# Optimization experiments

Measured on AMD Instinct MI355X. Metric: run time of the kernel, lower is better.

The kernel has to match this reference:

```python
import jax, jax.numpy as jnp
import numpy as np

HEADS = 24
HEAD_DIM = 128
HIDDEN = HEADS * HEAD_DIM          # 3072
MLP_DIM = int(HIDDEN * 4.0)        # 12288
EPS = 1e-6


def _layernorm(x, eps=EPS):
    mu = jnp.mean(x, axis=-1, keepdims=True)
    var = jnp.mean(jnp.square(x - mu), axis=-1, keepdims=True)
    return (x - mu) * jax.lax.rsqrt(var + eps)


def _rmsnorm(x, w, eps=EPS):
    var = jnp.mean(jnp.square(x), axis=-1, keepdims=True)
    return x * jax.lax.rsqrt(var + eps) * w


def _apply_rope_transposed(x, freqs_cis):
    # x: [B, S_img, H, Dh]; freqs_cis: [S_img, 2*Dh]
    cos, sin = jnp.split(freqs_cis[:, None, :], 2, axis=-1)  # each [S_img, 1, Dh]
    xr = x.reshape(*x.shape[:-1], -1, 2)                      # interleaved pairs
    x_real, x_imag = xr[..., 0], xr[..., 1]
    x_rot = jnp.stack([-x_imag, x_real], axis=-1).reshape(x.shape)
    return x * cos + x_rot * sin


def setup_inputs() -> dict:
    key = jax.random.key(0)
    ks = jax.random.split(key, 20)
    B, S_IMG, S_TXT = 1, 2048, 256
    s = 0.02
    inp = {
        "hidden_states": jax.random.normal(ks[0], (B, S_IMG, HIDDEN), jnp.float32),
        "encoder_hidden_states": jax.random.normal(ks[1], (B, S_TXT, HIDDEN), jnp.float32),
        "temb": jax.random.normal(ks[2], (B, HIDDEN), jnp.float32),
        "freqs_cis": jax.random.uniform(ks[3], (S_IMG, 2 * HEAD_DIM), jnp.float32),
        # AdaLN: Linear(hidden, 3*hidden)
        "w_norm": jax.random.normal(ks[4], (HIDDEN, 3 * HIDDEN), jnp.float32) * s,
        "b_norm": jnp.zeros((3 * HIDDEN,), jnp.float32),
        # attention projections (bias=True)
        "wq": jax.random.normal(ks[5], (HIDDEN, HIDDEN), jnp.float32) * s,
        "bq": jnp.zeros((HIDDEN,), jnp.float32),
        "wk": jax.random.normal(ks[6], (HIDDEN, HIDDEN), jnp.float32) * s,
        "bk": jnp.zeros((HIDDEN,), jnp.float32),
        "wv": jax.random.normal(ks[7], (HIDDEN, HIDDEN), jnp.float32) * s,
        "bv": jnp.zeros((HIDDEN,), jnp.float32),
        # QK RMSNorm weights over head_dim
        "nq_w": jnp.ones((HEAD_DIM,), jnp.float32),
        "nk_w": jnp.ones((HEAD_DIM,), jnp.float32),
        # parallel MLP branch
        "w_mlp": jax.random.normal(ks[8], (HIDDEN, MLP_DIM), jnp.float32) * s,
        "b_mlp": jnp.zeros((MLP_DIM,), jnp.float32),
        # proj_out: Linear(hidden + mlp_dim, hidden)
        "w_out": jax.random.normal(ks[9], (HIDDEN + MLP_DIM, HIDDEN), jnp.float32) * s,
        "b_out": jnp.zeros((HIDDEN,), jnp.float32),
    }
    return inp


def reference(hidden_states, encoder_hidden_states, temb, freqs_cis,
              w_norm, b_norm, wq, bq, wk, bk, wv, bv, nq_w, nk_w,
              w_mlp, b_mlp, w_out, b_out):
    B = hidden_states.shape[0]
    T = encoder_hidden_states.shape[1]  # text_seq_length

    x = jnp.concatenate([hidden_states, encoder_hidden_states], axis=1)  # [B,S,D]
    residual = x

    # AdaLayerNormZeroSingle
    emb = jax.nn.silu(temb) @ w_norm + b_norm          # [B, 3D]
    emb = emb[:, None, :]                              # [B, 1, 3D]
    shift, scale, gate = jnp.split(emb, 3, axis=-1)    # each [B,1,D]
    nx = _layernorm(x) * (1.0 + scale) + shift         # [B,S,D]

    # parallel MLP branch
    mlp = jax.nn.gelu(nx @ w_mlp + b_mlp, approximate=True)  # [B,S,MLP]

    # attention: q/k/v over full (img+txt) normed sequence
    q = (nx @ wq + bq).reshape(B, -1, HEADS, HEAD_DIM)
    k = (nx @ wk + bk).reshape(B, -1, HEADS, HEAD_DIM)
    v = (nx @ wv + bv).reshape(B, -1, HEADS, HEAD_DIM)
    q = _rmsnorm(q, nq_w)
    k = _rmsnorm(k, nk_w)

    # transposed RoPE on image tokens only
    q = jnp.concatenate([_apply_rope_transposed(q[:, :-T], freqs_cis), q[:, -T:]], axis=1)
    k = jnp.concatenate([_apply_rope_transposed(k[:, :-T], freqs_cis), k[:, -T:]], axis=1)

    # full (non-varlen) scaled dot-product attention
    scores = jnp.einsum("bqhd,bkhd->bhqk", q, k) / np.sqrt(HEAD_DIM).astype(np.float32)
    probs = jax.nn.softmax(scores, axis=-1)
    attn = jnp.einsum("bhqk,bkhd->bqhd", probs, v).reshape(B, -1, HIDDEN)

    # concat attention + mlp, project, gated residual
    h = jnp.concatenate([attn, mlp], axis=2)           # [B,S,D+MLP]
    h = gate * (h @ w_out + b_out) + residual          # [B,S,D]

    return h[:, :-T, :], h[:, -T:, :]
```

## Files before the change

### kernel.cpp

```cpp
#include <hip/hip_runtime.h>
#include <hip/hip_bf16.h>

typedef unsigned short u16;
typedef short s16x8 __attribute__((ext_vector_type(8)));
typedef float f32x4 __attribute__((ext_vector_type(4)));
typedef int   i32x4 __attribute__((ext_vector_type(4)));
typedef u16   u16x4 __attribute__((ext_vector_type(4)));
typedef unsigned int u32;
typedef u32   u32x2 __attribute__((ext_vector_type(2)));

#define HEADS  24
#define HD     128
#define HIDDEN 3072
#define MLPD   12288
#define NTOK   2304
#define SIMG   2048
#define NEMB   9216
#define CATD   15360
#define QKVD   9216
#define FUSEN  21504
#define LN_EPS 1e-6f
#define MB     9

__device__ __forceinline__ u16 f2us(float f){
  __hip_bfloat16 h = __float2bfloat16(f);
  return *reinterpret_cast<u16*>(&h);
}
__device__ __forceinline__ float us2f(u16 u){
  __hip_bfloat16 h;
  *reinterpret_cast<u16*>(&h) = u;
  return __bfloat162float(h);
}
__device__ __forceinline__ float gelu_tanh(float x){
  float y = 0.7978845608028654f*(x + 0.044715f*x*x*x);
  y = fminf(fmaxf(y, -12.f), 12.f);
  float e = __expf(-2.f*y);
  float t = (1.f - e) / (1.f + e);
  return 0.5f*x*(1.0f + t);
}
__device__ __forceinline__ void gload16(const u16* g, u16* l){
  __builtin_amdgcn_global_load_lds(
      (const __attribute__((address_space(1))) void*)g,
      (__attribute__((address_space(3))) void*)l, 16, 0, 0);
}
#define BAR() do{ asm volatile("":::"memory"); __builtin_amdgcn_s_barrier(); asm volatile("":::"memory"); }while(0)
#define LGKM0() asm volatile("s_waitcnt lgkmcnt(0)":::"memory")
#define VMW_(n) asm volatile("s_waitcnt vmcnt(" #n ")":::"memory")
#define VMW(n) VMW_(n)

__global__ __launch_bounds__(256)
void emb_partial(const float* __restrict__ temb, const float* __restrict__ wn,
                 float* __restrict__ partial)
{
  __shared__ float ls[384];
  int tid = threadIdx.x;
  int kb = blockIdx.y * 384;
  for (int i = tid; i < 384; i += 256){
    float t = temb[kb + i];
    ls[i] = t / (1.0f + __expf(-t));
  }
  __syncthreads();
  int j = blockIdx.x*256 + tid;
  const float* wp = wn + (size_t)kb*NEMB + j;
  float acc = 0.f;
  #pragma unroll 8
  for (int i = 0; i < 384; i++){ acc = fmaf(ls[i], wp[0], acc); wp += NEMB; }
  partial[blockIdx.y*NEMB + j] = acc;
}

__global__ __launch_bounds__(256)
void emb_reduce(const float* __restrict__ partial, const float* __restrict__ bn,
                float* __restrict__ emb)
{
  int j = blockIdx.x*256 + threadIdx.x;
  float s = bn[j];
  #pragma unroll
  for (int r = 0; r < 8; r++) s += partial[r*NEMB + j];
  emb[j] = s;
}

__global__ __launch_bounds__(256)
void ln_mod(const float* __restrict__ hs, const float* __restrict__ ehs,
            const float* __restrict__ emb, u16* __restrict__ nx)
{
  int row = blockIdx.x;
  const float* x = (row < SIMG) ? hs + (size_t)row*HIDDEN
                                : ehs + (size_t)(row - SIMG)*HIDDEN;
  int tid = threadIdx.x;
  float vals[12];
  float s = 0.f, ss = 0.f;
  #pragma unroll
  for (int i = 0; i < 3; i++){
    float4 v = *reinterpret_cast<const float4*>(x + i*1024 + tid*4);
    vals[i*4+0]=v.x; vals[i*4+1]=v.y; vals[i*4+2]=v.z; vals[i*4+3]=v.w;
    s += v.x+v.y+v.z+v.w;
    ss += v.x*v.x + v.y*v.y + v.z*v.z + v.w*v.w;
  }
  #pragma unroll
  for (int d = 1; d < 64; d <<= 1){ s += __shfl_xor(s, d); ss += __shfl_xor(ss, d); }
  __shared__ float red[8];
  if ((tid & 63) == 0){ red[tid>>6] = s; red[4 + (tid>>6)] = ss; }
  __syncthreads();
  s  = red[0]+red[1]+red[2]+red[3];
  ss = red[4]+red[5]+red[6]+red[7];
  float mu = s * (1.0f/HIDDEN);
  float var = ss * (1.0f/HIDDEN) - mu*mu;
  float rs = rsqrtf(var + LN_EPS);
  #pragma unroll
  for (int i = 0; i < 3; i++){
    int col = i*1024 + tid*4;
    u16x4 o;
    #pragma unroll
    for (int j = 0; j < 4; j++){
      float nv = (vals[i*4+j] - mu) * rs;
      float outv = nv * (1.0f + emb[HIDDEN + col + j]) + emb[col + j];
      o[j] = f2us(outv);
    }
    *reinterpret_cast<u16x4*>(nx + (size_t)row*HIDDEN + col) = o;
  }
}

__global__ __launch_bounds__(256)
void transpose_w(const float* __restrict__ W, u16* __restrict__ Wt,
                 int K, int N, int ldt, int noff)
{
  __shared__ float t[64][65];
  const int tid = threadIdx.x;
  const int kb = blockIdx.y * 64, nb = blockIdx.x * 64;
  #pragma unroll
  for (int i = 0; i < 4; i++){
    int row = (tid >> 4) + i*16;
    int c4  = (tid & 15) * 4;
    float4 v = *reinterpret_cast<const float4*>(W + (size_t)(kb+row)*N + nb + c4);
    t[row][c4] = v.x; t[row][c4+1] = v.y; t[row][c4+2] = v.z; t[row][c4+3] = v.w;
  }
  __syncthreads();
  int n  = tid >> 2;
  int kc = (tid & 3) * 16;
  u16 tmp[16];
  #pragma unroll
  for (int j = 0; j < 16; j++) tmp[j] = f2us(t[kc+j][n]);
  u16* dst = Wt + (size_t)(noff + nb + n)*ldt + kb + kc;
  *reinterpret_cast<i32x4*>(dst)     = *reinterpret_cast<const i32x4*>(tmp);
  *reinterpret_cast<i32x4*>(dst + 8) = *reinterpret_cast<const i32x4*>(tmp + 8);
}

template<int EPI>
__global__ __launch_bounds__(512, 2)
void gemm8(const u16* __restrict__ A_, int lda,
           const u16* __restrict__ Bt_, int ldb,
           int K, int N, int kspl,
           const float* __restrict__ b0, const float* __restrict__ b1,
           const float* __restrict__ b2, const float* __restrict__ b3,
           u16* __restrict__ qkvo, u16* __restrict__ hcat,
           float* __restrict__ outf)
{
  extern __shared__ __align__(16) u16 lds[];
  const int tid = threadIdx.x, lane = tid & 63, wid = tid >> 6;
  const int l15 = lane & 15, lhi = lane >> 4;
  const int wm = wid >> 2, wn = wid & 3;
  const int NKH = K / 32;

  const u16* Ag = A_  + (size_t)blockIdx.z * kspl;
  const u16* Bg = Bt_ + (size_t)blockIdx.z * kspl;

  const int nwg = gridDim.x;
  int orig = blockIdx.x;
  int qq = nwg >> 3, rr = nwg & 7;
  int xcd = orig & 7, loc = orig >> 3;
  int wg = (xcd < rr ? xcd*(qq+1) : rr*(qq+1) + (xcd-rr)*qq) + loc;
  const int m0 = (wg % MB) * 256;
  const int n0 = (wg / MB) * 256;

  const u16 *gA0, *gA1, *gB0, *gB1;
  {
    size_t offA[2], offB[2];
    #pragma unroll
    for (int q = 0; q < 2; q++){
      int Lb = q*8192 + tid*16;
      int r  = Lb >> 7;
      int gp = (Lb >> 4) & 7;
      int g  = gp ^ (r & 7);
      int row = 2*r + (g >> 2);
      int ke  = (g & 3) * 8;
      offA[q] = (size_t)(m0 + row)*lda + ke;
      offB[q] = (size_t)(n0 + row)*ldb + ke;
    }
    gA0 = Ag + offA[0]; gA1 = Ag + offA[1];
    gB0 = Bg + offB[0]; gB1 = Bg + offB[1];
  }
  u16* dA0 = lds + tid*8;
  u16* dA1 = lds + 4096 + tid*8;
  u16* dB0 = lds + 32768 + tid*8;
  u16* dB1 = lds + 36864 + tid*8;

  const char *pa0, *pb0;
  {
    const char* LB = (const char*)lds;
    int Ra = wm*128 + l15;
    pa0 = LB + (Ra>>1)*128 + (((((Ra&1)<<2)|lhi) ^ ((Ra>>1)&7))*16);
    int Rb = wn*64 + l15;
    pb0 = LB + 65536 + (Rb>>1)*128 + (((((Rb&1)<<2)|lhi) ^ ((Rb>>1)&7))*16);
  }

  f32x4 acc[8][4];
  #pragma unroll
  for (int i = 0; i < 8; i++)
    #pragma unroll
    for (int j = 0; j < 4; j++){ f32x4 z = {0.f,0.f,0.f,0.f}; acc[i][j] = z; }

  #define LD8(P_) (*reinterpret_cast<const s16x8*>(P_))
  #define MFMA_ALL(AF_, BF_) do{                                               \
    _Pragma("unroll") for (int a_=0;a_<8;a_++)                                 \
      _Pragma("unroll") for (int nf_=0;nf_<4;nf_++)                            \
        acc[a_][nf_] = __builtin_amdgcn_mfma_f32_16x16x32_bf16(                \
            (AF_)[a_], (BF_)[nf_], acc[a_][nf_], 0, 0, 0); }while(0)

  #define PHASEP(RP_,SP_,DOI_,GOFF_,VN_) do{                                   \
    s16x8 af[8], bf[4];                                                        \
    af[0] = LD8(pa0 + (RP_)*16384);                                            \
    _Pragma("unroll") for (int i_=0;i_<4;i_++)                                 \
      bf[i_] = LD8(pb0 + (RP_)*16384 + i_*1024);                               \
    _Pragma("unroll") for (int i_=1;i_<8;i_++)                                 \
      af[i_] = LD8(pa0 + (RP_)*16384 + (i_>>2)*4096 + (i_&3)*1024);            \
    if (DOI_){                                                                 \
      gload16(gA0+(GOFF_), dA0+(SP_)*8192); gload16(gA1+(GOFF_), dA1+(SP_)*8192);\
      gload16(gB0+(GOFF_), dB0+(SP_)*8192); gload16(gB1+(GOFF_), dB1+(SP_)*8192);\
    }                                                                          \
    __builtin_amdgcn_s_setprio(1);                                             \
    MFMA_ALL(af, bf);                                                          \
    __builtin_amdgcn_s_setprio(0);                                             \
    LGKM0();                                                                   \
    VMW(VN_);                                                                  \
    BAR();                                                                     \
  }while(0)

  gload16(gA0,    dA0);        gload16(gA1,    dA1);
  gload16(gB0,    dB0);        gload16(gB1,    dB1);
  gload16(gA0+32, dA0+8192);   gload16(gA1+32, dA1+8192);
  gload16(gB0+32, dB0+8192);   gload16(gB1+32, dB1+8192);
  gload16(gA0+64, dA0+16384);  gload16(gA1+64, dA1+16384);
  gload16(gB0+64, dB0+16384);  gload16(gB1+64, dB1+16384);
  VMW(8);
  BAR();

  const int nblk = NKH >> 3;
  for (int b = 0; b < nblk - 1; b++){
    PHASEP(0,3,1, 96,8); PHASEP(1,0,1,128,8); PHASEP(2,1,1,160,8); PHASEP(3,2,1,192,8);
    PHASEP(0,3,1,224,8); PHASEP(1,0,1,256,8); PHASEP(2,1,1,288,8); PHASEP(3,2,1,320,8);
    gA0 += 256; gA1 += 256; gB0 += 256; gB1 += 256;
  }
  PHASEP(0,3,1, 96,8); PHASEP(1,0,1,128,8); PHASEP(2,1,1,160,8); PHASEP(3,2,1,192,8);
  PHASEP(0,3,1,224,8); PHASEP(1,0,0,  0,4); PHASEP(2,1,0,  0,0); PHASEP(3,2,0,  0,0);

  #undef PHASEP
  #undef MFMA_ALL
  #undef LD8

  #pragma unroll
  for (int a = 0; a < 8; a++){
    #pragma unroll
    for (int nf = 0; nf < 4; nf++){
      int col = n0 + wn*64 + nf*16 + l15;
      #pragma unroll
      for (int r = 0; r < 4; r++){
        int row = m0 + wm*128 + a*16 + lhi*4 + r;
        float v = acc[a][nf][r];
        if constexpr (EPI == 0){
          if (col < QKVD){
            const float* bp = b0; int c = col;
            if (c >= 6144){ bp = b2; c -= 6144; }
            else if (c >= 3072){ bp = b1; c -= 3072; }
            qkvo[(size_t)row*QKVD + col] = f2us(v + bp[c]);
          } else {
            int c2 = col - QKVD;
            hcat[(size_t)row*CATD + HIDDEN + c2] = f2us(gelu_tanh(v + b3[c2]));
          }
        } else {
          outf[(size_t)blockIdx.z*NTOK*HIDDEN + (size_t)row*HIDDEN + col] = v;
        }
      }
    }
  }
}

__global__ __launch_bounds__(256)
void reduce_out(const float* __restrict__ part, const float* __restrict__ bout,
                const float* __restrict__ emb,
                const float* __restrict__ hs, const float* __restrict__ ehs,
                float* __restrict__ outp)
{
  int row = blockIdx.x;
  const float* res = (row < SIMG) ? hs + (size_t)row*HIDDEN
                                  : ehs + (size_t)(row - SIMG)*HIDDEN;
  #pragma unroll
  for (int i = 0; i < 3; i++){
    int col = i*1024 + threadIdx.x*4;
    float4 a = *reinterpret_cast<const float4*>(part + (size_t)row*HIDDEN + col);
    float4 b = *reinterpret_cast<const float4*>(part + (size_t)NTOK*HIDDEN + (size_t)row*HIDDEN + col);
    float4 rr = *reinterpret_cast<const float4*>(res + col);
    float4 bb = *reinterpret_cast<const float4*>(bout + col);
    float4 gg = *reinterpret_cast<const float4*>(emb + 2*HIDDEN + col);
    float4 o;
    o.x = gg.x*(a.x+b.x+bb.x) + rr.x;
    o.y = gg.y*(a.y+b.y+bb.y) + rr.y;
    o.z = gg.z*(a.z+b.z+bb.z) + rr.z;
    o.w = gg.w*(a.w+b.w+bb.w) + rr.w;
    *reinterpret_cast<float4*>(outp + (size_t)row*HIDDEN + col) = o;
  }
}

__global__ __launch_bounds__(256)
void qk_post(u16* __restrict__ qkv,
             const float* __restrict__ nqw, const float* __restrict__ nkw,
             const float* __restrict__ fc)
{
  int rid = blockIdx.x*4 + (threadIdx.x >> 6);
  int lane = threadIdx.x & 63;
  int isK = rid >= NTOK*HEADS;
  int r = isK ? rid - NTOK*HEADS : rid;
  int token = r / HEADS, head = r % HEADS;
  u16* p = qkv + (size_t)token*QKVD + (isK ? HIDDEN : 0) + head*HD + lane*2;
  unsigned int u = *reinterpret_cast<unsigned int*>(p);
  float v0 = us2f((u16)(u & 0xffff));
  float v1 = us2f((u16)(u >> 16));
  float ss = v0*v0 + v1*v1;
  #pragma unroll
  for (int d = 1; d < 64; d <<= 1) ss += __shfl_xor(ss, d);
  float rs = rsqrtf(ss * (1.0f/HD) + LN_EPS);
  const float* wv = isK ? nkw : nqw;
  v0 *= rs * wv[lane*2];
  v1 *= rs * wv[lane*2+1];
  if (token < SIMG){
    const float* f = fc + (size_t)token*(2*HD);
    float c0 = f[lane*2],      c1 = f[lane*2+1];
    float s0 = f[HD + lane*2], s1 = f[HD + lane*2+1];
    float o0 = v0*c0 - v1*s0;
    float o1 = v1*c1 + v0*s1;
    v0 = o0; v1 = o1;
  }
  unsigned int uo = (unsigned int)f2us(v0) | ((unsigned int)f2us(v1) << 16);
  *reinterpret_cast<unsigned int*>(p) = uo;
}

__global__ __launch_bounds__(256)
void attn_kernel(const u16* __restrict__ qkv, u16* __restrict__ hcat)
{
  __shared__ __align__(16) u16 Qs[64][136];
  __shared__ __align__(16) u16 Ks[64][136];
  __shared__ __align__(16) u16 Vt[128][72];
  __shared__ __align__(16) u16 Ps[64][72];

  const int tid = threadIdx.x, lane = tid & 63, w = tid >> 6;
  const int head = blockIdx.y, qb = blockIdx.x;
  const int l15 = lane & 15, lhi = lane >> 4;
  const int q0 = qb * 64;
  const float scale = 0.08838834764831845f;

  #pragma unroll
  for (int i = 0; i < 4; i++){
    int c = tid + 256*i;
    int row = c >> 4, d0 = (c & 15) * 8;
    i32x4 vv = *reinterpret_cast<const i32x4*>(qkv + (size_t)(q0+row)*QKVD + head*HD + d0);
    *reinterpret_cast<i32x4*>(&Qs[row][d0]) = vv;
  }

  int krow[4], kd0[4];
  #pragma unroll
  for (int i = 0; i < 4; i++){ int c = tid + 256*i; krow[i] = c >> 4; kd0[i] = (c & 15)*8; }
  const int vbase = w*16 + lhi*4;
  const int vd0   = l15*8;
  char* vwp = (char*)(&Vt[0][0]) + vd0*144 + (((vbase>>3) ^ ((vd0>>3)&7))*16) + (vbase&7)*2;

  i32x4 kr0, kr1, kr2, kr3, vr0, vr1, vr2, vr3;
  {
    const u16* kbp = qkv + HIDDEN + (size_t)head*HD;
    const u16* vbp = qkv + 2*HIDDEN + (size_t)head*HD;
    kr0 = *reinterpret_cast<const i32x4*>(kbp + (size_t)(krow[0])*QKVD + kd0[0]);
    kr1 = *reinterpret_cast<const i32x4*>(kbp + (size_t)(krow[1])*QKVD + kd0[1]);
    kr2 = *reinterpret_cast<const i32x4*>(kbp + (size_t)(krow[2])*QKVD + kd0[2]);
    kr3 = *reinterpret_cast<const i32x4*>(kbp + (size_t)(krow[3])*QKVD + kd0[3]);
    vr0 = *reinterpret_cast<const i32x4*>(vbp + (size_t)(vbase+0)*QKVD + vd0);
    vr1 = *reinterpret_cast<const i32x4*>(vbp + (size_t)(vbase+1)*QKVD + vd0);
    vr2 = *reinterpret_cast<const i32x4*>(vbp + (size_t)(vbase+2)*QKVD + vd0);
    vr3 = *reinterpret_cast<const i32x4*>(vbp + (size_t)(vbase+3)*QKVD + vd0);
  }
  __syncthreads();

  s16x8 qf[4];
  #pragma unroll
  for (int ks = 0; ks < 4; ks++)
    qf[ks] = *reinterpret_cast<const s16x8*>(&Qs[w*16 + l15][ks*32 + lhi*8]);

  f32x4 O[8];
  #pragma unroll
  for (int i = 0; i < 8; i++){ f32x4 z = {0.f,0.f,0.f,0.f}; O[i] = z; }
  float mrow[4], lrow[4];
  #pragma unroll
  for (int r = 0; r < 4; r++){ mrow[r] = -1e30f; lrow[r] = 0.f; }

  for (int kv0 = 0; kv0 < NTOK; kv0 += 64){
    *reinterpret_cast<i32x4*>(&Ks[krow[0]][kd0[0]]) = kr0;
    *reinterpret_cast<i32x4*>(&Ks[krow[1]][kd0[1]]) = kr1;
    *reinterpret_cast<i32x4*>(&Ks[krow[2]][kd0[2]]) = kr2;
    *reinterpret_cast<i32x4*>(&Ks[krow[3]][kd0[3]]) = kr3;
    #pragma unroll
    for (int dd = 0; dd < 8; dd++){
      u32 a0 = (u32)(dd & 1 ? ((u32)vr0[dd>>1]) >> 16 : ((u32)vr0[dd>>1]) & 0xffff);
      u32 a1 = (u32)(dd & 1 ? ((u32)vr1[dd>>1]) >> 16 : ((u32)vr1[dd>>1]) & 0xffff);
      u32 a2 = (u32)(dd & 1 ? ((u32)vr2[dd>>1]) >> 16 : ((u32)vr2[dd>>1]) & 0xffff);
      u32 a3 = (u32)(dd & 1 ? ((u32)vr3[dd>>1]) >> 16 : ((u32)vr3[dd>>1]) & 0xffff);
      u32x2 pk; pk[0] = a0 | (a1 << 16); pk[1] = a2 | (a3 << 16);
      *reinterpret_cast<u32x2*>(vwp + dd*144) = pk;
    }
    __syncthreads();

    if (kv0 + 64 < NTOK){
      const u16* kbp = qkv + (size_t)(kv0+64)*QKVD + HIDDEN + (size_t)head*HD;
      const u16* vbp = qkv + (size_t)(kv0+64)*QKVD + 2*HIDDEN + (size_t)head*HD;
      kr0 = *reinterpret_cast<const i32x4*>(kbp + (size_t)(krow[0])*QKVD + kd0[0]);
      kr1 = *reinterpret_cast<const i32x4*>(kbp + (size_t)(krow[1])*QKVD + kd0[1]);
      kr2 = *reinterpret_cast<const i32x4*>(kbp + (size_t)(krow[2])*QKVD + kd0[2]);
      kr3 = *reinterpret_cast<const i32x4*>(kbp + (size_t)(krow[3])*QKVD + kd0[3]);
      vr0 = *reinterpret_cast<const i32x4*>(vbp + (size_t)(vbase+0)*QKVD + vd0);
      vr1 = *reinterpret_cast<const i32x4*>(vbp + (size_t)(vbase+1)*QKVD + vd0);
      vr2 = *reinterpret_cast<const i32x4*>(vbp + (size_t)(vbase+2)*QKVD + vd0);
      vr3 = *reinterpret_cast<const i32x4*>(vbp + (size_t)(vbase+3)*QKVD + vd0);
    }

    f32x4 S[4];
    #pragma unroll
    for (int nf = 0; nf < 4; nf++){ f32x4 z = {0.f,0.f,0.f,0.f}; S[nf] = z; }
    #pragma unroll
    for (int ks = 0; ks < 4; ks++){
      #pragma unroll
      for (int nf = 0; nf < 4; nf++){
        s16x8 b = *reinterpret_cast<const s16x8*>(&Ks[nf*16 + l15][ks*32 + lhi*8]);
        S[nf] = __builtin_amdgcn_mfma_f32_16x16x32_bf16(qf[ks], b, S[nf], 0, 0, 0);
      }
    }
    #pragma unroll
    for (int nf = 0; nf < 4; nf++)
      #pragma unroll
      for (int r = 0; r < 4; r++) S[nf][r] *= scale;

    float fsc[4];
    #pragma unroll
    for (int r = 0; r < 4; r++){
      float mx = -1e30f;
      #pragma unroll
      for (int nf = 0; nf < 4; nf++) mx = fmaxf(mx, S[nf][r]);
      #pragma unroll
      for (int d = 1; d < 16; d <<= 1) mx = fmaxf(mx, __shfl_xor(mx, d));
      float mn = fmaxf(mrow[r], mx);
      float f = __expf(mrow[r] - mn);
      mrow[r] = mn; fsc[r] = f;
      float lsum = 0.f;
      int prow = w*16 + lhi*4 + r;
      #pragma unroll
      for (int nf = 0; nf < 4; nf++){
        float pvl = __expf(S[nf][r] - mn);
        lsum += pvl;
        int pcol = nf*16 + l15;
        int col = (((pcol>>3) ^ (prow&7)) << 3) | (pcol & 7);
        Ps[prow][col] = f2us(pvl);
      }
      #pragma unroll
      for (int d = 1; d < 16; d <<= 1) lsum += __shfl_xor(lsum, d);
      lrow[r] = lrow[r]*f + lsum;
    }
    #pragma unroll
    for (int nf = 0; nf < 8; nf++)
      #pragma unroll
      for (int r = 0; r < 4; r++) O[nf][r] *= fsc[r];

    #pragma unroll
    for (int ks = 0; ks < 2; ks++){
      int prow = w*16 + l15;
      int cb = ((ks*4 + lhi) ^ (prow & 7)) << 3;
      s16x8 a = *reinterpret_cast<const s16x8*>(&Ps[prow][cb]);
      #pragma unroll
      for (int nf = 0; nf < 8; nf++){
        int d = nf*16 + l15;
        int vb = ((ks*4 + lhi) ^ ((d>>3)&7)) << 3;
        s16x8 b = *reinterpret_cast<const s16x8*>(&Vt[d][vb]);
        O[nf] = __builtin_amdgcn_mfma_f32_16x16x32_bf16(a, b, O[nf], 0, 0, 0);
      }
    }
    __syncthreads();
  }

  #pragma unroll
  for (int nf = 0; nf < 8; nf++){
    #pragma unroll
    for (int r = 0; r < 4; r++){
      int row = q0 + w*16 + lhi*4 + r;
      int col = head*HD + nf*16 + l15;
      hcat[(size_t)row*CATD + col] = f2us(O[nf][r] / lrow[r]);
    }
  }
}

extern "C" void kernel_launch(void* const* d_in, const int* in_sizes, int n_in,
                              void* d_out, int out_size, void* d_ws, size_t ws_size,
                              hipStream_t stream)
{
  const float* hs    = (const float*)d_in[0];
  const float* ehs   = (const float*)d_in[1];
  const float* temb  = (const float*)d_in[2];
  const float* fc    = (const float*)d_in[3];
  const float* wnorm = (const float*)d_in[4];
  const float* bnorm = (const float*)d_in[5];
  const float* wq    = (const float*)d_in[6];
  const float* bq    = (const float*)d_in[7];
  const float* wk    = (const float*)d_in[8];
  const float* bk    = (const float*)d_in[9];
  const float* wv    = (const float*)d_in[10];
  const float* bv    = (const float*)d_in[11];
  const float* nqw   = (const float*)d_in[12];
  const float* nkw   = (const float*)d_in[13];
  const float* wmlp  = (const float*)d_in[14];
  const float* bmlp  = (const float*)d_in[15];
  const float* wout  = (const float*)d_in[16];
  const float* bout  = (const float*)d_in[17];
  float* outp = (float*)d_out;

  char* ws = (char*)d_ws;
  float* emb  = (float*)ws;
  float* part = (float*)(ws + 36864);
  u16* nx     = (u16*)(ws + 36864 + 294912);
  u16* qkv    = nx  + (size_t)NTOK*HIDDEN;
  u16* hcat   = qkv + (size_t)NTOK*QKVD;
  u16* Wt     = hcat + (size_t)NTOK*CATD;
  float* partial = (float*)nx;

  hipFuncSetAttribute((const void*)gemm8<0>, hipFuncAttributeMaxDynamicSharedMemorySize, 131072);
  hipFuncSetAttribute((const void*)gemm8<1>, hipFuncAttributeMaxDynamicSharedMemorySize, 131072);

  emb_partial<<<dim3(36,8), 256, 0, stream>>>(temb, wnorm, part);
  emb_reduce<<<36, 256, 0, stream>>>(part, bnorm, emb);
  ln_mod<<<NTOK, 256, 0, stream>>>(hs, ehs, emb, nx);

  transpose_w<<<dim3(48,48), 256, 0, stream>>>(wq,   Wt, HIDDEN, HIDDEN, HIDDEN, 0);
  transpose_w<<<dim3(48,48), 256, 0, stream>>>(wk,   Wt, HIDDEN, HIDDEN, HIDDEN, HIDDEN);
  transpose_w<<<dim3(48,48), 256, 0, stream>>>(wv,   Wt, HIDDEN, HIDDEN, HIDDEN, 2*HIDDEN);
  transpose_w<<<dim3(192,48), 256, 0, stream>>>(wmlp, Wt, HIDDEN, MLPD, HIDDEN, QKVD);

  gemm8<0><<<dim3((FUSEN/256)*MB, 1, 1), 512, 131072, stream>>>(
      nx, HIDDEN, Wt, HIDDEN, HIDDEN, FUSEN, 0,
      bq, bk, bv, bmlp, qkv, hcat, nullptr);

  transpose_w<<<dim3(48,240), 256, 0, stream>>>(wout, Wt, CATD, HIDDEN, CATD, 0);

  qk_post<<<(2*NTOK*HEADS)/4, 256, 0, stream>>>(qkv, nqw, nkw, fc);
  attn_kernel<<<dim3(NTOK/64, HEADS), 256, 0, stream>>>(qkv, hcat);

  gemm8<1><<<dim3((HIDDEN/256)*MB, 1, 2), 512, 131072, stream>>>(
      hcat, CATD, Wt, CATD, CATD/2, HIDDEN, CATD/2,
      nullptr, nullptr, nullptr, nullptr, nullptr, nullptr, partial);

  reduce_out<<<NTOK, 256, 0, stream>>>(partial, bout, emb, hs, ehs, outp);
}
```

Baseline: 968.5 us.

## Enlarge attention query tile to 128 rows with 8 waves sharing K/V tiles

The attention kernel now processes 128 query rows per block using 512 threads (8 waves), so each K/V tile loaded into shared memory is reused by twice as many queries. The per-thread K/V global loads are halved and the V transpose writes are resized to match. Q fragments are loaded straight from global memory into registers, which removes the Q shared buffer and a barrier. The grid shrinks to 18x24 blocks, which may lower occupancy or load balance on a GPU with many compute units. The diff does not show whether the hidden softmax/PV code was updated for the doubled Ps buffer and wave count.

Result: no change. 952.3 us (-1.7%).

```diff
diff --git a/kernel.cpp b/kernel.cpp
--- a/kernel.cpp
+++ b/kernel.cpp
@@ -5,6 +5,7 @@
 typedef short s16x8 __attribute__((ext_vector_type(8)));
 typedef float f32x4 __attribute__((ext_vector_type(4)));
 typedef int   i32x4 __attribute__((ext_vector_type(4)));
+typedef int   i32x2 __attribute__((ext_vector_type(2)));
 typedef u16   u16x4 __attribute__((ext_vector_type(4)));
 typedef unsigned int u32;
 typedef u32   u32x2 __attribute__((ext_vector_type(2)));
@@ -343,54 +344,46 @@
   *reinterpret_cast<unsigned int*>(p) = uo;
 }
 
-__global__ __launch_bounds__(256)
+__global__ __launch_bounds__(512)
 void attn_kernel(const u16* __restrict__ qkv, u16* __restrict__ hcat)
 {
-  __shared__ __align__(16) u16 Qs[64][136];
   __shared__ __align__(16) u16 Ks[64][136];
   __shared__ __align__(16) u16 Vt[128][72];
-  __shared__ __align__(16) u16 Ps[64][72];
+  __shared__ __align__(16) u16 Ps[128][72];
 
   const int tid = threadIdx.x, lane = tid & 63, w = tid >> 6;
-  const int head = blockIdx.y, qb = blockIdx.x;
+  const int head = blockIdx.y;
   const int l15 = lane & 15, lhi = lane >> 4;
-  const int q0 = qb * 64;
+  const int q0 = blockIdx.x * 128;
   const float scale = 0.08838834764831845f;
 
-  #pragma unroll
-  for (int i = 0; i < 4; i++){
-    int c = tid + 256*i;
-    int row = c >> 4, d0 = (c & 15) * 8;
-    i32x4 vv = *reinterpret_cast<const i32x4*>(qkv + (size_t)(q0+row)*QKVD + head*HD + d0);
-    *reinterpret_cast<i32x4*>(&Qs[row][d0]) = vv;
-  }
-
-  int krow[4], kd0[4];
-  #pragma unroll
-  for (int i = 0; i < 4; i++){ int c = tid + 256*i; krow[i] = c >> 4; kd0[i] = (c & 15)*8; }
-  const int vbase = w*16 + lhi*4;
-  const int vd0   = l15*8;
+  s16x8 qf[4];
+  {
+    const u16* qrow = qkv + (size_t)(q0 + w*16 + l15)*QKVD + head*HD;
+    #pragma unroll
+    for (int ks = 0; ks < 4; ks++)
+      qf[ks] = *reinterpret_cast<const s16x8*>(qrow + ks*32 + lhi*8);
+  }
+
+  int krow[2], kd0[2];
+  #pragma unroll
+  for (int i = 0; i < 2; i++){ int c = tid + 512*i; krow[i] = c >> 4; kd0[i] = (c & 15)*8; }
+  const int vd0   = (tid & 31) * 4;
+  const int vbase = (tid >> 5) * 4;
   char* vwp = (char*)(&Vt[0][0]) + vd0*144 + (((vbase>>3) ^ ((vd0>>3)&7))*16) + (vbase&7)*2;
 
-  i32x4 kr0, kr1, kr2, kr3, vr0, vr1, vr2, vr3;
+  i32x4 kr0, kr1;
+  i32x2 vr0, vr1, vr2, vr3;
   {
     const u16* kbp = qkv + HIDDEN + (size_t)head*HD;
     const u16* vbp = qkv + 2*HIDDEN + (size_t)head*HD;
     kr0 = *reinterpret_cast<const i32x4*>(kbp + (size_t)(krow[0])*QKVD + kd0[0]);
     kr1 = *reinterpret_cast<const i32x4*>(kbp + (size_t)(krow[1])*QKVD + kd0[1]);
-    kr2 = *reinterpret_cast<const i32x4*>(kbp + (size_t)(krow[2])*QKVD + kd0[2]);
-    kr3 = *reinterpret_cast<const i32x4*>(kbp + (size_t)(krow[3])*QKVD + kd0[3]);
-    vr0 = *reinterpret_cast<const i32x4*>(vbp + (size_t)(vbase+0)*QKVD + vd0);
-    vr1 = *reinterpret_cast<const i32x4*>(vbp + (size_t)(vbase+1)*QKVD + vd0);
-    vr2 = *reinterpret_cast<const i32x4*>(vbp + (size_t)(vbase+2)*QKVD + vd0);
-    vr3 = *reinterpret_cast<const i32x4*>(vbp + (size_t)(vbase+3)*QKVD + vd0);
-  }
-  __syncthreads();
-
-  s16x8 qf[4];
-  #pragma unroll
-  for (int ks = 0; ks < 4; ks++)
-    qf[ks] = *reinterpret_cast<const s16x8*>(&Qs[w*16 + l15][ks*32 + lhi*8]);
+    vr0 = *reinterpret_cast<const i32x2*>(vbp + (size_t)(vbase+0)*QKVD + vd0);
+    vr1 = *reinterpret_cast<const i32x2*>(vbp + (size_t)(vbase+1)*QKVD + vd0);
+    vr2 = *reinterpret_cast<const i32x2*>(vbp + (size_t)(vbase+2)*QKVD + vd0);
+    vr3 = *reinterpret_cast<const i32x2*>(vbp + (size_t)(vbase+3)*QKVD + vd0);
+  }
 
   f32x4 O[8];
   #pragma unroll
@@ -402,10 +395,8 @@
   for (int kv0 = 0; kv0 < NTOK; kv0 += 64){
     *reinterpret_cast<i32x4*>(&Ks[krow[0]][kd0[0]]) = kr0;
     *reinterpret_cast<i32x4*>(&Ks[krow[1]][kd0[1]]) = kr1;
-    *reinterpret_cast<i32x4*>(&Ks[krow[2]][kd0[2]]) = kr2;
-    *reinterpret_cast<i32x4*>(&Ks[krow[3]][kd0[3]]) = kr3;
-    #pragma unroll
-    for (int dd = 0; dd < 8; dd++){
+    #pragma unroll
+    for (int dd = 0; dd < 4; dd++){
       u32 a0 = (u32)(dd & 1 ? ((u32)vr0[dd>>1]) >> 16 : ((u32)vr0[dd>>1]) & 0xffff);
       u32 a1 = (u32)(dd & 1 ? ((u32)vr1[dd>>1]) >> 16 : ((u32)vr1[dd>>1]) & 0xffff);
       u32 a2 = (u32)(dd & 1 ? ((u32)vr2[dd>>1]) >> 16 : ((u32)vr2[dd>>1]) & 0xffff);
@@ -420,12 +411,10 @@
       const u16* vbp = qkv + (size_t)(kv0+64)*QKVD + 2*HIDDEN + (size_t)head*HD;
       kr0 = *reinterpret_cast<const i32x4*>(kbp + (size_t)(krow[0])*QKVD + kd0[0]);
       kr1 = *reinterpret_cast<const i32x4*>(kbp + (size_t)(krow[1])*QKVD + kd0[1]);
-      kr2 = *reinterpret_cast<const i32x4*>(kbp + (size_t)(krow[2])*QKVD + kd0[2]);
-      kr3 = *reinterpret_cast<const i32x4*>(kbp + (size_t)(krow[3])*QKVD + kd0[3]);
-      vr0 = *reinterpret_cast<const i32x4*>(vbp + (size_t)(vbase+0)*QKVD + vd0);
-      vr1 = *reinterpret_cast<const i32x4*>(vbp + (size_t)(vbase+1)*QKVD + vd0);
-      vr2 = *reinterpret_cast<const i32x4*>(vbp + (size_t)(vbase+2)*QKVD + vd0);
-      vr3 = *reinterpret_cast<const i32x4*>(vbp + (size_t)(vbase+3)*QKVD + vd0);
+      vr0 = *reinterpret_cast<const i32x2*>(vbp + (size_t)(vbase+0)*QKVD + vd0);
+      vr1 = *reinterpret_cast<const i32x2*>(vbp + (size_t)(vbase+1)*QKVD + vd0);
+      vr2 = *reinterpret_cast<const i32x2*>(vbp + (size_t)(vbase+2)*QKVD + vd0);
+      vr3 = *reinterpret_cast<const i32x2*>(vbp + (size_t)(vbase+3)*QKVD + vd0);
     }
 
     f32x4 S[4];
@@ -553,7 +542,7 @@
   transpose_w<<<dim3(48,240), 256, 0, stream>>>(wout, Wt, CATD, HIDDEN, CATD, 0);
 
   qk_post<<<(2*NTOK*HEADS)/4, 256, 0, stream>>>(qkv, nqw, nkw, fc);
-  attn_kernel<<<dim3(NTOK/64, HEADS), 256, 0, stream>>>(qkv, hcat);
+  attn_kernel<<<dim3(NTOK/128, HEADS), 512, 0, stream>>>(qkv, hcat);
 
   gemm8<1><<<dim3((HIDDEN/256)*MB, 1, 2), 512, 131072, stream>>>(
       hcat, CATD, Wt, CATD, CATD/2, HIDDEN, CATD/2,
```
